# Optimization experiments

Hardware: AMD Instinct MI355X
Metric: run time of the kernel (lower is better)

Reference implementation:

```python
import jax, jax.numpy as jnp
import numpy as np

N_NODES = 100000
N_EDGES = 1250000
IN_DIM = 6
HID = 64


def gcn_conv(x, W, b, src, dst, deg_inv_sqrt):
    # x: [N, F_in] -> [N, F_out]; symmetric-normalized aggregation with self-loops
    h = x @ W  # [N, F_out]
    norm = deg_inv_sqrt[src] * deg_inv_sqrt[dst]  # [E]
    msg = h[src] * norm[:, None]                  # gather + scale, [E, F_out]
    agg = jax.ops.segment_sum(msg, dst, num_segments=x.shape[0])
    # self-loop contribution: norm = deg_inv_sqrt[i]^2 = 1/deg[i]
    out = agg + h * (deg_inv_sqrt ** 2)[:, None] + b
    return out


def setup_inputs() -> dict:
    key = jax.random.key(0)
    ks = jax.random.split(key, 8)
    x = jax.random.normal(ks[0], (N_NODES, IN_DIM), dtype=jnp.float32)
    edge_index = jax.random.randint(ks[1], (2, N_EDGES), 0, N_NODES, dtype=jnp.int64)
    s1 = 1.0 / np.sqrt(IN_DIM)
    s2 = 1.0 / np.sqrt(HID)
    W1 = jax.random.uniform(ks[2], (IN_DIM, HID), jnp.float32, -s1, s1)
    b1 = jnp.zeros((HID,), jnp.float32)
    W2 = jax.random.uniform(ks[3], (HID, HID), jnp.float32, -s2, s2)
    b2 = jnp.zeros((HID,), jnp.float32)
    Wfc = jax.random.uniform(ks[4], (HID, 1), jnp.float32, -s2, s2)
    bfc = jnp.zeros((1,), jnp.float32)
    return {"x": x, "edge_index": edge_index, "W1": W1, "b1": b1,
            "W2": W2, "b2": b2, "Wfc": Wfc, "bfc": bfc}


def reference(x, edge_index, W1, b1, W2, b2, Wfc, bfc):
    src, dst = edge_index[0], edge_index[1]
    n = x.shape[0]
    # degree with self-loops (GCN default): in-degree at destination + 1
    deg = jax.ops.segment_sum(jnp.ones((src.shape[0],), x.dtype), dst, num_segments=n) + 1.0
    deg_inv_sqrt = jax.lax.rsqrt(deg)
    h = gcn_conv(x, W1, b1, src, dst, deg_inv_sqrt)
    h = jax.nn.relu(h)
    h = gcn_conv(h, W2, b2, src, dst, deg_inv_sqrt)
    g = h.mean(axis=0)              # [HID] graph readout
    out = jax.nn.sigmoid(g @ Wfc + bfc)  # [1]
    return out
```

## Files before the change

kernel.cpp:

```cpp
#include <hip/hip_runtime.h>
#include <math.h>

#define N_NODES 100000
#define N_EDGES 1250000
#define IN_DIM 6
#define HID 64

#define BIN_SHIFT 8
#define BIN_NODES 256
#define NBIN 391
#define A_BLOCKS 250
#define EPB (N_EDGES / A_BLOCKS)
#define CAP 4096
#define SOFF (NBIN * CAP)

__device__ inline float lo16(unsigned u) { return __uint_as_float(u << 16); }
__device__ inline float hi16(unsigned u) { return __uint_as_float(u & 0xffff0000u); }
__device__ inline unsigned short f2bf(float f) {
    unsigned u = __float_as_uint(f);
    u += 0x7FFFu + ((u >> 16) & 1u);
    return (unsigned short)(u >> 16);
}
__device__ inline unsigned pack2(float a, float b) {
    return (unsigned)f2bf(a) | ((unsigned)f2bf(b) << 16);
}

__global__ __launch_bounds__(1024) void binFill(const int* __restrict__ src,
                                                const int* __restrict__ dst,
                                                int* __restrict__ cnt,
                                                unsigned* __restrict__ rec) {
    __shared__ int lc[2 * NBIN];
    __shared__ int lb[2 * NBIN];
    int t = threadIdx.x;
    for (int i = t; i < 2 * NBIN; i += 1024) lc[i] = 0;
    __syncthreads();
    int base = blockIdx.x * EPB;
    for (int i0 = t * 4; i0 < EPB; i0 += 4096) {
        int4 d4 = *(const int4*)&dst[base + i0];
        int4 s4 = *(const int4*)&src[base + i0];
        atomicAdd(&lc[d4.x >> BIN_SHIFT], 1);
        atomicAdd(&lc[d4.y >> BIN_SHIFT], 1);
        atomicAdd(&lc[d4.z >> BIN_SHIFT], 1);
        atomicAdd(&lc[d4.w >> BIN_SHIFT], 1);
        atomicAdd(&lc[NBIN + (s4.x >> BIN_SHIFT)], 1);
        atomicAdd(&lc[NBIN + (s4.y >> BIN_SHIFT)], 1);
        atomicAdd(&lc[NBIN + (s4.z >> BIN_SHIFT)], 1);
        atomicAdd(&lc[NBIN + (s4.w >> BIN_SHIFT)], 1);
    }
    __syncthreads();
    for (int i = t; i < 2 * NBIN; i += 1024) {
        int c = lc[i];
        int off = (c > 0) ? atomicAdd(&cnt[i], c) : 0;
        int bin = (i < NBIN) ? i : (i - NBIN);
        int region = (i < NBIN) ? bin * CAP : SOFF + bin * CAP;
        lb[i] = region + off;
        lc[i] = 0;
    }
    __syncthreads();
    for (int i0 = t * 4; i0 < EPB; i0 += 4096) {
        int4 d4 = *(const int4*)&dst[base + i0];
        int4 s4 = *(const int4*)&src[base + i0];
        int bD0 = d4.x >> BIN_SHIFT, bD1 = d4.y >> BIN_SHIFT;
        int bD2 = d4.z >> BIN_SHIFT, bD3 = d4.w >> BIN_SHIFT;
        int p0 = lb[bD0] + atomicAdd(&lc[bD0], 1);
        int p1 = lb[bD1] + atomicAdd(&lc[bD1], 1);
        int p2 = lb[bD2] + atomicAdd(&lc[bD2], 1);
        int p3 = lb[bD3] + atomicAdd(&lc[bD3], 1);
        rec[p0] = ((unsigned)(d4.x & (BIN_NODES - 1)) << 17) | (unsigned)s4.x;
        rec[p1] = ((unsigned)(d4.y & (BIN_NODES - 1)) << 17) | (unsigned)s4.y;
        rec[p2] = ((unsigned)(d4.z & (BIN_NODES - 1)) << 17) | (unsigned)s4.z;
        rec[p3] = ((unsigned)(d4.w & (BIN_NODES - 1)) << 17) | (unsigned)s4.w;
        int bS0 = NBIN + (s4.x >> BIN_SHIFT), bS1 = NBIN + (s4.y >> BIN_SHIFT);
        int bS2 = NBIN + (s4.z >> BIN_SHIFT), bS3 = NBIN + (s4.w >> BIN_SHIFT);
        int q0 = lb[bS0] + atomicAdd(&lc[bS0], 1);
        int q1 = lb[bS1] + atomicAdd(&lc[bS1], 1);
        int q2 = lb[bS2] + atomicAdd(&lc[bS2], 1);
        int q3 = lb[bS3] + atomicAdd(&lc[bS3], 1);
        rec[q0] = ((unsigned)(s4.x & (BIN_NODES - 1)) << 17) | (unsigned)d4.x;
        rec[q1] = ((unsigned)(s4.y & (BIN_NODES - 1)) << 17) | (unsigned)d4.y;
        rec[q2] = ((unsigned)(s4.z & (BIN_NODES - 1)) << 17) | (unsigned)d4.z;
        rec[q3] = ((unsigned)(s4.w & (BIN_NODES - 1)) << 17) | (unsigned)d4.w;
    }
}

__global__ __launch_bounds__(1024) void disXH(const unsigned* __restrict__ rec,
                                              const int* __restrict__ cnt,
                                              const float* __restrict__ x,
                                              int* __restrict__ deg,
                                              float* __restrict__ dis,
                                              uint4* __restrict__ xpad) {
    __shared__ int histS[4][BIN_NODES];
    int t = threadIdx.x, g = t >> 8;
    if (t < 4 * BIN_NODES) ((int*)histS)[t] = 0;
    __syncthreads();
    int bin = blockIdx.x;
    int beg = bin * CAP, end = beg + cnt[bin];
    for (int j = beg + t; j < end; j += 1024) atomicAdd(&histS[g][rec[j] >> 17], 1);
    __syncthreads();
    if (t < BIN_NODES) {
        int n = (bin << BIN_SHIFT) + t;
        if (n < N_NODES) {
            int h = histS[0][t] + histS[1][t] + histS[2][t] + histS[3][t];
            deg[n] = h;
            float d = rsqrtf((float)h + 1.0f);
            dis[n] = d;
            float2 xa = *(const float2*)&x[n * IN_DIM + 0];
            float2 xb = *(const float2*)&x[n * IN_DIM + 2];
            float2 xc = *(const float2*)&x[n * IN_DIM + 4];
            uint4 u;
            u.x = pack2(xa.x * d, xa.y * d);
            u.y = pack2(xb.x * d, xb.y * d);
            u.z = pack2(xc.x * d, xc.y * d);
            u.w = 0;
            xpad[n] = u;
        }
    }
}

__global__ __launch_bounds__(1024) void aggW(const unsigned* __restrict__ rec,
                                             const int* __restrict__ cnt,
                                             const int* __restrict__ deg,
                                             const float* __restrict__ dis,
                                             const uint4* __restrict__ xpad,
                                             const float* __restrict__ W1,
                                             const float* __restrict__ b1,
                                             float* __restrict__ vsum) {
    __shared__ unsigned srcL[CAP];
    __shared__ float wlS[4][BIN_NODES];
    __shared__ int degL[BIN_NODES];
    __shared__ int startS[BIN_NODES];
    __shared__ int cur[BIN_NODES];
    __shared__ int sc[BIN_NODES];
    __shared__ float sAll[BIN_NODES][8];
    __shared__ float w1s[IN_DIM * HID];
    __shared__ float b1s[HID];
    __shared__ float vpart[HID];
    int t = threadIdx.x, g = t >> 8;
    int bin = blockIdx.x;

    if (t < 4 * BIN_NODES) ((float*)wlS)[t] = 0.f;
    if (t < IN_DIM * HID) w1s[t] = W1[t];
    if (t >= 1024 - HID) { int c = t - (1024 - HID); b1s[c] = b1[c]; vpart[c] = 0.f; }
    __syncthreads();

    {
        int beg = SOFF + bin * CAP, end = beg + cnt[NBIN + bin];
        for (int j = beg + t; j < end; j += 1024) {
            unsigned r = rec[j];
            atomicAdd(&wlS[g][r >> 17], dis[r & 131071u]);
        }
    }
    __syncthreads();

    if (t < BIN_NODES) {
        int n = (bin << BIN_SHIFT) + t;
        int h = (n < N_NODES) ? deg[n] : 0;
        degL[t] = h;
        sc[t] = h;
        float d = (n < N_NODES) ? rsqrtf((float)h + 1.0f) : 0.f;
        float wloc = wlS[0][t] + wlS[1][t] + wlS[2][t] + wlS[3][t];
        sAll[t][6] = d;
        sAll[t][7] = (n < N_NODES) ? d * (wloc + d) : 0.f;
    }
    __syncthreads();
    for (int off = 1; off < BIN_NODES; off <<= 1) {
        int add = 0;
        if (t < BIN_NODES && t >= off) add = sc[t - off];
        __syncthreads();
        if (t < BIN_NODES) sc[t] += add;
        __syncthreads();
    }
    if (t < BIN_NODES) {
        int st = sc[t] - degL[t];
        startS[t] = st;
        cur[t] = st;
    }
    __syncthreads();

    {
        int beg = bin * CAP, end = beg + cnt[bin];
        for (int j = beg + t; j < end; j += 1024) {
            unsigned r = rec[j];
            int pos = atomicAdd(&cur[r >> 17], 1);
            if (pos < CAP) srcL[pos] = r & 131071u;
        }
    }
    __syncthreads();

    {
        int node = t >> 2, sub = t & 3;
        int st = startS[node], cn = degL[node];
        int lim = min(st + cn, CAP);
        float s0 = 0.f, s1 = 0.f, s2 = 0.f, s3 = 0.f, s4 = 0.f, s5 = 0.f;
        for (int k = st + sub; k < lim; k += 4) {
            uint4 px = xpad[srcL[k]];
            s0 += lo16(px.x); s1 += hi16(px.x);
            s2 += lo16(px.y); s3 += hi16(px.y);
            s4 += lo16(px.z); s5 += hi16(px.z);
        }
        s0 += __shfl_xor(s0, 1, 64); s0 += __shfl_xor(s0, 2, 64);
        s1 += __shfl_xor(s1, 1, 64); s1 += __shfl_xor(s1, 2, 64);
        s2 += __shfl_xor(s2, 1, 64); s2 += __shfl_xor(s2, 2, 64);
        s3 += __shfl_xor(s3, 1, 64); s3 += __shfl_xor(s3, 2, 64);
        s4 += __shfl_xor(s4, 1, 64); s4 += __shfl_xor(s4, 2, 64);
        s5 += __shfl_xor(s5, 1, 64); s5 += __shfl_xor(s5, 2, 64);
        if (sub == 0) {
            int n = (bin << BIN_SHIFT) + node;
            if (n < N_NODES) {
                uint4 px = xpad[n];
                s0 += lo16(px.x); s1 += hi16(px.x);
                s2 += lo16(px.y); s3 += hi16(px.y);
                s4 += lo16(px.z); s5 += hi16(px.z);
            }
            sAll[node][0] = s0; sAll[node][1] = s1; sAll[node][2] = s2;
            sAll[node][3] = s3; sAll[node][4] = s4; sAll[node][5] = s5;
        }
    }
    __syncthreads();

    {
        int c = t & 63, grp = t >> 6;
        float v = 0.f;
#pragma unroll
        for (int i = 0; i < 16; ++i) {
            int node = grp * 16 + i;
            float d = sAll[node][6], cw = sAll[node][7];
            float a = sAll[node][0] * w1s[0 * HID + c]
                    + sAll[node][1] * w1s[1 * HID + c]
                    + sAll[node][2] * w1s[2 * HID + c]
                    + sAll[node][3] * w1s[3 * HID + c]
                    + sAll[node][4] * w1s[4 * HID + c]
                    + sAll[node][5] * w1s[5 * HID + c];
            v += cw * fmaxf(d * a + b1s[c], 0.f);
        }
        atomicAdd(&vpart[c], v);
    }
    __syncthreads();
    if (t < HID) atomicAdd(&vsum[t], vpart[t]);
}

__global__ void finalK(const float* __restrict__ vsum, const float* __restrict__ W2,
                       const float* __restrict__ b2, const float* __restrict__ Wfc,
                       const float* __restrict__ bfc, float* __restrict__ out) {
    __shared__ float vL[HID];
    int t = threadIdx.x;
    vL[t] = vsum[t] * (1.0f / N_NODES);
    __syncthreads();
    float g = b2[t];
    for (int k = 0; k < HID; ++k) g += vL[k] * W2[k * HID + t];
    float z = g * Wfc[t];
    for (int off = 32; off > 0; off >>= 1) z += __shfl_down(z, off, 64);
    if (t == 0) out[0] = 1.0f / (1.0f + expf(-(z + bfc[0])));
}

extern "C" void kernel_launch(void* const* d_in, const int* in_sizes, int n_in,
                              void* d_out, int out_size, void* d_ws, size_t ws_size,
                              hipStream_t stream) {
    const float* x   = (const float*)d_in[0];
    const int*   ei  = (const int*)d_in[1];
    const float* W1  = (const float*)d_in[2];
    const float* b1  = (const float*)d_in[3];
    const float* W2  = (const float*)d_in[4];
    const float* b2  = (const float*)d_in[5];
    const float* Wfc = (const float*)d_in[6];
    const float* bfc = (const float*)d_in[7];
    const int* src = ei;
    const int* dst = ei + N_EDGES;

    char* ws = (char*)d_ws;
    size_t off = 0;
    auto alloc = (+[](char* base, size_t* o, size_t bytes) {
        char* p = base + *o;
        *o += (bytes + 255) & ~(size_t)255;
        return p;
    });
    int*      cnt  = (int*)     alloc(ws, &off, (size_t)2 * NBIN * 4);
    float*    vsum = (float*)   alloc(ws, &off, 64 * 4);
    uint4*    xpad = (uint4*)   alloc(ws, &off, (size_t)N_NODES * 16);
    float*    dis  = (float*)   alloc(ws, &off, (size_t)N_NODES * 4);
    int*      deg  = (int*)     alloc(ws, &off, (size_t)N_NODES * 4);
    unsigned* rec  = (unsigned*)alloc(ws, &off, (size_t)2 * SOFF * 4);

    hipMemsetAsync(cnt, 0, ((size_t)2 * NBIN * 4 + 255 & ~(size_t)255) + 64 * 4, stream);

    binFill<<<A_BLOCKS, 1024, 0, stream>>>(src, dst, cnt, rec);
    disXH<<<NBIN, 1024, 0, stream>>>(rec, cnt, x, deg, dis, xpad);
    aggW<<<NBIN, 1024, 0, stream>>>(rec, cnt, deg, dis, xpad, W1, b1, vsum);
    finalK<<<1, 64, 0, stream>>>(vsum, W2, b2, Wfc, bfc, (float*)d_out);
}
```

Baseline: 124.9 us.

## Stage binned edge records in LDS before coalesced global writeout

The binFill kernel now keeps its edges in registers instead of reading them twice from global memory. It runs a local histogram and a wave prefix scan separately for the dst and src binnings, sorts records by bin in shared memory, and then writes them to global memory in index order. Records of the same bin land in contiguous global addresses, which replaces the scattered per-edge global stores. In exchange it uses about 40KB of LDS per block, runs two passes with more barriers, and clamps positions defensively.

```diff
diff --git a/kernel.cpp b/kernel.cpp
--- a/kernel.cpp
+++ b/kernel.cpp
@@ -29,58 +29,131 @@
                                                 const int* __restrict__ dst,
                                                 int* __restrict__ cnt,
                                                 unsigned* __restrict__ rec) {
-    __shared__ int lc[2 * NBIN];
-    __shared__ int lb[2 * NBIN];
+    __shared__ int lc[NBIN];
+    __shared__ int scv[NBIN];
+    __shared__ int lb[NBIN];
+    __shared__ int lbase[NBIN];
+    __shared__ unsigned ldsRec[EPB];
+    __shared__ int ldsPos[EPB];
+
     int t = threadIdx.x;
-    for (int i = t; i < 2 * NBIN; i += 1024) lc[i] = 0;
-    __syncthreads();
     int base = blockIdx.x * EPB;
-    for (int i0 = t * 4; i0 < EPB; i0 += 4096) {
-        int4 d4 = *(const int4*)&dst[base + i0];
-        int4 s4 = *(const int4*)&src[base + i0];
-        atomicAdd(&lc[d4.x >> BIN_SHIFT], 1);
-        atomicAdd(&lc[d4.y >> BIN_SHIFT], 1);
-        atomicAdd(&lc[d4.z >> BIN_SHIFT], 1);
-        atomicAdd(&lc[d4.w >> BIN_SHIFT], 1);
-        atomicAdd(&lc[NBIN + (s4.x >> BIN_SHIFT)], 1);
-        atomicAdd(&lc[NBIN + (s4.y >> BIN_SHIFT)], 1);
-        atomicAdd(&lc[NBIN + (s4.z >> BIN_SHIFT)], 1);
-        atomicAdd(&lc[NBIN + (s4.w >> BIN_SHIFT)], 1);
-    }
-    __syncthreads();
-    for (int i = t; i < 2 * NBIN; i += 1024) {
-        int c = lc[i];
-        int off = (c > 0) ? atomicAdd(&cnt[i], c) : 0;
-        int bin = (i < NBIN) ? i : (i - NBIN);
-        int region = (i < NBIN) ? bin * CAP : SOFF + bin * CAP;
-        lb[i] = region + off;
-        lc[i] = 0;
-    }
-    __syncthreads();
-    for (int i0 = t * 4; i0 < EPB; i0 += 4096) {
-        int4 d4 = *(const int4*)&dst[base + i0];
-        int4 s4 = *(const int4*)&src[base + i0];
-        int bD0 = d4.x >> BIN_SHIFT, bD1 = d4.y >> BIN_SHIFT;
-        int bD2 = d4.z >> BIN_SHIFT, bD3 = d4.w >> BIN_SHIFT;
-        int p0 = lb[bD0] + atomicAdd(&lc[bD0], 1);
-        int p1 = lb[bD1] + atomicAdd(&lc[bD1], 1);
-        int p2 = lb[bD2] + atomicAdd(&lc[bD2], 1);
-        int p3 = lb[bD3] + atomicAdd(&lc[bD3], 1);
-        rec[p0] = ((unsigned)(d4.x & (BIN_NODES - 1)) << 17) | (unsigned)s4.x;
-        rec[p1] = ((unsigned)(d4.y & (BIN_NODES - 1)) << 17) | (unsigned)s4.y;
-        rec[p2] = ((unsigned)(d4.z & (BIN_NODES - 1)) << 17) | (unsigned)s4.z;
-        rec[p3] = ((unsigned)(d4.w & (BIN_NODES - 1)) << 17) | (unsigned)s4.w;
-        int bS0 = NBIN + (s4.x >> BIN_SHIFT), bS1 = NBIN + (s4.y >> BIN_SHIFT);
-        int bS2 = NBIN + (s4.z >> BIN_SHIFT), bS3 = NBIN + (s4.w >> BIN_SHIFT);
-        int q0 = lb[bS0] + atomicAdd(&lc[bS0], 1);
-        int q1 = lb[bS1] + atomicAdd(&lc[bS1], 1);
-        int q2 = lb[bS2] + atomicAdd(&lc[bS2], 1);
-        int q3 = lb[bS3] + atomicAdd(&lc[bS3], 1);
-        rec[q0] = ((unsigned)(s4.x & (BIN_NODES - 1)) << 17) | (unsigned)d4.x;
-        rec[q1] = ((unsigned)(s4.y & (BIN_NODES - 1)) << 17) | (unsigned)d4.y;
-        rec[q2] = ((unsigned)(s4.z & (BIN_NODES - 1)) << 17) | (unsigned)d4.z;
-        rec[q3] = ((unsigned)(s4.w & (BIN_NODES - 1)) << 17) | (unsigned)d4.w;
-    }
+
+    int4 dA = *(const int4*)&dst[base + t * 4];
+    int4 sA = *(const int4*)&src[base + t * 4];
+    const int TB = (EPB - 4096) / 4;
+    bool hasB = (t < TB);
+    int4 dB = make_int4(0, 0, 0, 0), sB = make_int4(0, 0, 0, 0);
+    if (hasB) {
+        dB = *(const int4*)&dst[base + 4096 + t * 4];
+        sB = *(const int4*)&src[base + 4096 + t * 4];
+    }
+
+#define HIST4(v4) do {                                  \
+        atomicAdd(&lc[(v4).x >> BIN_SHIFT], 1);         \
+        atomicAdd(&lc[(v4).y >> BIN_SHIFT], 1);         \
+        atomicAdd(&lc[(v4).z >> BIN_SHIFT], 1);         \
+        atomicAdd(&lc[(v4).w >> BIN_SHIFT], 1);         \
+    } while (0)
+
+#define SCAT1(key, val) do {                                                  \
+        int b_ = (key) >> BIN_SHIFT;                                          \
+        int loc_ = lbase[b_] + atomicAdd(&lc[b_], 1);                         \
+        loc_ = min(loc_, EPB - 1);                                            \
+        ldsRec[loc_] = ((unsigned)((key) & (BIN_NODES - 1)) << 17)            \
+                     | (unsigned)(val);                                       \
+        ldsPos[loc_] = lb[b_] + (loc_ - lbase[b_]);                           \
+    } while (0)
+
+#define SCAT4(k4, v4) do {                  \
+        SCAT1((k4).x, (v4).x);              \
+        SCAT1((k4).y, (v4).y);              \
+        SCAT1((k4).z, (v4).z);              \
+        SCAT1((k4).w, (v4).w);              \
+    } while (0)
+
+#define WRITEOUT() do {                                                       \
+        for (int i = t; i < EPB; i += 1024) {                                 \
+            unsigned p_ = (unsigned)ldsPos[i];                                \
+            if (p_ < (unsigned)(2 * SOFF)) rec[p_] = ldsRec[i];               \
+        }                                                                     \
+    } while (0)
+
+    if (t < NBIN) lc[t] = 0;
+    __syncthreads();
+    HIST4(dA);
+    if (hasB) HIST4(dB);
+    __syncthreads();
+    if (t < NBIN) {
+        int c = lc[t];
+        scv[t] = c;
+        lc[t] = 0;
+        int off = (c > 0) ? atomicAdd(&cnt[t], c) : 0;
+        lb[t] = t * CAP + off;
+    }
+    __syncthreads();
+    if (t < 64) {
+        int carry = 0;
+#pragma unroll
+        for (int cb = 0; cb < NBIN; cb += 64) {
+            int idx = cb + t;
+            int c = (idx < NBIN) ? scv[idx] : 0;
+            int v = c;
+#pragma unroll
+            for (int off = 1; off < 64; off <<= 1) {
+                int u = __shfl_up(v, off, 64);
+                if (t >= off) v += u;
+            }
+            if (idx < NBIN) lbase[idx] = carry + v - c;
+            carry += __shfl(v, 63, 64);
+        }
+    }
+    __syncthreads();
+    SCAT4(dA, sA);
+    if (hasB) SCAT4(dB, sB);
+    __syncthreads();
+    WRITEOUT();
+    __syncthreads();
+
+    if (t < NBIN) lc[t] = 0;
+    __syncthreads();
+    HIST4(sA);
+    if (hasB) HIST4(sB);
+    __syncthreads();
+    if (t < NBIN) {
+        int c = lc[t];
+        scv[t] = c;
+        lc[t] = 0;
+        int off = (c > 0) ? atomicAdd(&cnt[NBIN + t], c) : 0;
+        lb[t] = SOFF + t * CAP + off;
+    }
+    __syncthreads();
+    if (t < 64) {
+        int carry = 0;
+#pragma unroll
+        for (int cb = 0; cb < NBIN; cb += 64) {
+            int idx = cb + t;
+            int c = (idx < NBIN) ? scv[idx] : 0;
+            int v = c;
+#pragma unroll
+            for (int off = 1; off < 64; off <<= 1) {
+                int u = __shfl_up(v, off, 64);
+                if (t >= off) v += u;
+            }
+            if (idx < NBIN) lbase[idx] = carry + v - c;
+            carry += __shfl(v, 63, 64);
+        }
+    }
+    __syncthreads();
+    SCAT4(sA, dA);
+    if (hasB) SCAT4(sB, dB);
+    __syncthreads();
+    WRITEOUT();
+
+#undef HIST4
+#undef SCAT1
+#undef SCAT4
+#undef WRITEOUT
 }
 
 __global__ __launch_bounds__(1024) void disXH(const unsigned* __restrict__ rec,
```

Result: no change. 124.0 us (median of 2 runs) (-0.7%).
